# Kernel tuning notes

Measured on AMD Instinct MI355X. Metric: run time of the kernel, lower is better.

## Reference

```python
import jax, jax.numpy as jnp
import numpy as np

SIZES = [6890, 1723, 431, 108, 27]
P = [s + 1 for s in SIZES]  # padding vertex at each level
SPIRAL = 9
ENC_IN = [3, 16, 32, 64]; ENC_OUT = [16, 32, 64, 128]
DEC_IN = [128, 64, 32, 32, 16]; DEC_OUT = [64, 32, 32, 16, 3]
LATENT = 128
B = 64


def setup_inputs() -> dict:
    ks = iter(jax.random.split(jax.random.key(0), 80))
    def nrm(shape, scale=1.0):
        return jax.random.normal(next(ks), shape, dtype=jnp.float32) * scale
    inp = {'x': nrm((B, P[0], 3))}
    for l in range(4):
        inp['S%d' % l] = jax.random.randint(next(ks), (P[l], SPIRAL), 0, P[l], dtype=jnp.int32)
        inp['D%d' % l] = nrm((P[l + 1], P[l]), float(1.0 / np.sqrt(P[l])))
        inp['U%d' % l] = nrm((P[l], P[l + 1]), float(1.0 / np.sqrt(P[l + 1])))
    for i, (ci, co) in enumerate(zip(ENC_IN, ENC_OUT)):
        inp['W_e%d' % i] = nrm((ci * SPIRAL, co), float(1.0 / np.sqrt(ci * SPIRAL)))
        inp['b_e%d' % i] = nrm((co,), 0.02)
    inp['W_fe'] = nrm((P[4] * ENC_OUT[-1], LATENT), float(1.0 / np.sqrt(P[4] * ENC_OUT[-1])))
    inp['b_fe'] = nrm((LATENT,), 0.02)
    inp['W_fd'] = nrm((LATENT, P[4] * DEC_IN[0]), float(1.0 / np.sqrt(LATENT)))
    inp['b_fd'] = nrm((P[4] * DEC_IN[0],), 0.02)
    for i, (ci, co) in enumerate(zip(DEC_IN, DEC_OUT)):
        inp['W_d%d' % i] = nrm((ci * SPIRAL, co), float(1.0 / np.sqrt(ci * SPIRAL)))
        inp['b_d%d' % i] = nrm((co,), 0.02)
    return inp


def _sconv(x, idx, W, b, act):
    # spiral gather: x[B,P,F], idx[P,S] -> [B,P,S*F]; Linear + activation + zero last (padding) vertex
    Bn, Pn, F = x.shape
    g = x[:, idx, :].reshape(Bn, Pn, -1)
    y = act(g @ W + b)
    return y.at[:, -1, :].set(0.0)


def _forward(x, S, D, U, We, be, W_fe, b_fe, W_fd, b_fd, Wd, bd):
    elu = jax.nn.elu
    h = x
    for i in range(4):  # encoder: spiral conv then downsample
        h = _sconv(h, S[i], We[i], be[i], elu)
        h = jnp.einsum('pq,bqf->bpf', D[i], h)
    z = h.reshape(h.shape[0], -1) @ W_fe + b_fe
    h = (z @ W_fd + b_fd).reshape(z.shape[0], P[4], DEC_IN[0])
    for i in range(4):  # decoder: upsample then spiral conv
        h = jnp.einsum('pq,bqf->bpf', U[3 - i], h)
        h = _sconv(h, S[3 - i], Wd[i], bd[i], elu)
    h = _sconv(h, S[0], Wd[4], bd[4], lambda v: v)  # final identity-activation conv to xyz
    return h, z


def reference(x, S0, S1, S2, S3, D0, D1, D2, D3, U0, U1, U2, U3,
              W_e0, b_e0, W_e1, b_e1, W_e2, b_e2, W_e3, b_e3,
              W_fe, b_fe, W_fd, b_fd,
              W_d0, b_d0, W_d1, b_d1, W_d2, b_d2, W_d3, b_d3, W_d4, b_d4):
    return _forward(x, [S0, S1, S2, S3], [D0, D1, D2, D3], [U0, U1, U2, U3],
                    [W_e0, W_e1, W_e2, W_e3], [b_e0, b_e1, b_e2, b_e3],
                    W_fe, b_fe, W_fd, b_fd,
                    [W_d0, W_d1, W_d2, W_d3, W_d4], [b_d0, b_d1, b_d2, b_d3, b_d4])
```

## Files before the change

kernel.cpp:

```cpp
#include <hip/hip_runtime.h>
#include <math.h>

typedef unsigned short u16;
typedef _Float16 f16;
typedef __attribute__((ext_vector_type(8))) _Float16 f16x8;
typedef __attribute__((ext_vector_type(4))) float f32x4;
typedef float4 __attribute__((aligned(4))) float4u;

constexpr int P0 = 6891, P1 = 1724, P2 = 432, P3 = 109, P4 = 28;
constexpr int P0p = 6912;

constexpr size_t OFF_ZB   = 0;
constexpr size_t OFF_MD0  = OFF_ZB   + 256;
constexpr size_t OFF_MU0  = OFF_MD0  + (size_t)1792 * 6912 * 2;
constexpr size_t OFF_MD1  = OFF_MU0  + (size_t)6912 * 1792 * 2;
constexpr size_t OFF_MU1  = OFF_MD1  + (size_t)512 * 1792 * 2;
constexpr size_t OFF_MD2  = OFF_MU1  + (size_t)1792 * 512 * 2;
constexpr size_t OFF_MU2  = OFF_MD2  + (size_t)128 * 512 * 2;
constexpr size_t OFF_MD3  = OFF_MU2  + (size_t)512 * 128 * 2;
constexpr size_t OFF_MU3  = OFF_MD3  + (size_t)128 * 128 * 2;
constexpr size_t OFF_WE1  = OFF_MU3  + (size_t)128 * 128 * 2;
constexpr size_t OFF_WE2  = OFF_WE1  + (size_t)32 * 192 * 2;
constexpr size_t OFF_WE3  = OFF_WE2  + (size_t)64 * 320 * 2;
constexpr size_t OFF_WD0  = OFF_WE3  + (size_t)128 * 576 * 2;
constexpr size_t OFF_WD1  = OFF_WD0  + (size_t)64 * 1152 * 2;
constexpr size_t OFF_WD2  = OFF_WD1  + (size_t)32 * 576 * 2;
constexpr size_t OFF_WD3  = OFF_WD2  + (size_t)32 * 320 * 2;
constexpr size_t OFF_WT0  = OFF_WD3  + (size_t)16 * 320 * 2;
constexpr size_t OFF_XT   = OFF_WT0  + (size_t)16 * 128 * 2;
constexpr size_t OFF_FCP  = OFF_XT   + (size_t)6912 * 64 * 8 * 2;
constexpr size_t OFF_B0   = OFF_FCP  + (size_t)28 * 8192 * 4;
constexpr size_t OFF_B1   = OFF_B0   + (size_t)1024 * 6912 * 2;
constexpr size_t OFF_PB   = OFF_B1   + (size_t)6912 * 2048 * 2;
constexpr size_t OFF_END  = OFF_PB   + (size_t)14680064;

constexpr int CN_MD0 = 1792 * 864, CN_MU0 = 6912 * 224, CN_MD1 = 512 * 224,
              CN_MU1 = 1792 * 64, CN_MD2 = 128 * 64, CN_MU2 = 512 * 16,
              CN_MD3 = 128 * 16, CN_MU3 = 128 * 16,
              CN_W1 = 32 * 24, CN_W2 = 64 * 40, CN_W3 = 128 * 72,
              CN_V0 = 64 * 144, CN_V1 = 32 * 72, CN_V2 = 32 * 40, CN_V3 = 16 * 40,
              CN_W0 = 16 * 16, CN_XT = 6912 * 64, CN_ZB = 32;
constexpr int CN_TOTAL = CN_MD0 + CN_MU0 + CN_MD1 + CN_MU1 + CN_MD2 + CN_MU2 +
                         CN_MD3 + CN_MU3 + CN_W1 + CN_W2 + CN_W3 + CN_V0 + CN_V1 +
                         CN_V2 + CN_V3 + CN_W0 + CN_XT + CN_ZB;

__device__ __forceinline__ u16 f2h(float v) {
  f16 h = (f16)v;
  return __builtin_bit_cast(u16, h);
}
__device__ __forceinline__ float h2f(u16 u) {
  return (float)__builtin_bit_cast(f16, u);
}
__device__ __forceinline__ float eluf(float v) { return v > 0.f ? v : expm1f(v); }

__device__ __forceinline__ void gload16(const void* g, void* lds) {
  __builtin_amdgcn_global_load_lds(
      (const __attribute__((address_space(1))) unsigned int*)g,
      (__attribute__((address_space(3))) unsigned int*)lds, 16, 0, 0);
}

struct PrepSrc {
  const float *D0, *U0, *D1, *U1, *D2, *U2, *D3, *U3;
  const float *We1, *We2, *We3, *Wd0, *Wd1, *Wd2, *Wd3;
  const float *We0, *x;
};

__device__ __forceinline__ void conv_m_item(const float* __restrict__ M, u16* __restrict__ out,
                                            int idx, int P, int Q, int Qpad) {
  int cpr = Qpad >> 3;
  int p = idx / cpr, cq = idx - p * cpr;
  int w0 = (cq << 3) & ~63;
  int q0 = w0 + (((cq & 7) ^ (p & 7)) << 3);
  uint4 pk;
  if (p < P && q0 + 8 <= Q) {
    const float* s = M + (size_t)p * Q + q0;
    float4 va = *(const float4u*)s;
    float4 vb = *(const float4u*)(s + 4);
    pk.x = f2h(va.x) | ((unsigned)f2h(va.y) << 16);
    pk.y = f2h(va.z) | ((unsigned)f2h(va.w) << 16);
    pk.z = f2h(vb.x) | ((unsigned)f2h(vb.y) << 16);
    pk.w = f2h(vb.z) | ((unsigned)f2h(vb.w) << 16);
  } else {
    u16 v[8];
#pragma unroll
    for (int j = 0; j < 8; ++j) {
      int q = q0 + j;
      float f = (p < P && q < Q) ? M[(size_t)p * Q + q] : 0.f;
      v[j] = f2h(f);
    }
    pk.x = v[0] | ((unsigned)v[1] << 16); pk.y = v[2] | ((unsigned)v[3] << 16);
    pk.z = v[4] | ((unsigned)v[5] << 16); pk.w = v[6] | ((unsigned)v[7] << 16);
  }
  *(uint4*)(out + ((size_t)idx << 3)) = pk;
}

__device__ __forceinline__ void conv_w_item(const float* __restrict__ W, u16* __restrict__ out,
                                            int idx, int K, int F, int Kpad) {
  int cpr = Kpad >> 3;
  int co = idx / cpr, ck = idx - co * cpr;
  int w0 = (ck << 3) & ~63;
  int k0 = w0 + (((ck & 7) ^ (co & 7)) << 3);
  u16 v[8];
#pragma unroll
  for (int j = 0; j < 8; ++j) {
    int k = k0 + j;
    float f = (k < K) ? W[(size_t)k * F + co] : 0.f;
    v[j] = f2h(f);
  }
  uint4 pk;
  pk.x = v[0] | ((unsigned)v[1] << 16); pk.y = v[2] | ((unsigned)v[3] << 16);
  pk.z = v[4] | ((unsigned)v[5] << 16); pk.w = v[6] | ((unsigned)v[7] << 16);
  *(uint4*)(out + ((size_t)idx << 3)) = pk;
}

__device__ __forceinline__ void conv_w0_item(const float* __restrict__ W, u16* __restrict__ out,
                                             int idx) {
  int co = idx >> 4, ck = idx & 15;
  int w0 = (ck << 3) & ~63;
  int k0 = w0 + (((ck & 7) ^ (co & 7)) << 3);
  u16 v[8];
#pragma unroll
  for (int j = 0; j < 8; ++j) {
    int k = k0 + j;
    int s = k >> 3, c = k & 7;
    float f = (s < 9 && c < 3) ? W[(size_t)(s * 3 + c) * 16 + co] : 0.f;
    v[j] = f2h(f);
  }
  uint4 pk;
  pk.x = v[0] | ((unsigned)v[1] << 16); pk.y = v[2] | ((unsigned)v[3] << 16);
  pk.z = v[4] | ((unsigned)v[5] << 16); pk.w = v[6] | ((unsigned)v[7] << 16);
  *(uint4*)(out + ((size_t)idx << 3)) = pk;
}

__global__ __launch_bounds__(256) void kprep(PrepSrc a, char* __restrict__ ws) {
  int i = blockIdx.x * 256 + threadIdx.x;
  if (i >= CN_TOTAL) return;
  if (i < CN_MD0) { conv_m_item(a.D0, (u16*)(ws + OFF_MD0), i, P1, P0, 6912); return; }
  i -= CN_MD0;
  if (i < CN_MU0) { conv_m_item(a.U0, (u16*)(ws + OFF_MU0), i, P0, P1, 1792); return; }
  i -= CN_MU0;
  if (i < CN_XT) {
    u16* xt = (u16*)(ws + OFF_XT);
    int p = i >> 6, b = i & 63;
    float v0 = 0, v1 = 0, v2 = 0;
    if (p < P0) { const float* s = a.x + ((size_t)b * P0 + p) * 3; v0 = s[0]; v1 = s[1]; v2 = s[2]; }
    uint4 pk;
    pk.x = f2h(v0) | ((unsigned)f2h(v1) << 16);
    pk.y = f2h(v2);
    pk.z = 0; pk.w = 0;
    *(uint4*)(xt + ((size_t)i << 3)) = pk;
    return;
  }
  i -= CN_XT;
  if (i < CN_MD1) { conv_m_item(a.D1, (u16*)(ws + OFF_MD1), i, P2, P1, 1792); return; }
  i -= CN_MD1;
  if (i < CN_MU1) { conv_m_item(a.U1, (u16*)(ws + OFF_MU1), i, P1, P2, 512); return; }
  i -= CN_MU1;
  if (i < CN_MD2) { conv_m_item(a.D2, (u16*)(ws + OFF_MD2), i, P3, P2, 512); return; }
  i -= CN_MD2;
  if (i < CN_MU2) { conv_m_item(a.U2, (u16*)(ws + OFF_MU2), i, P2, P3, 128); return; }
  i -= CN_MU2;
  if (i < CN_MD3) { conv_m_item(a.D3, (u16*)(ws + OFF_MD3), i, P4, P3, 128); return; }
  i -= CN_MD3;
  if (i < CN_MU3) { conv_m_item(a.U3, (u16*)(ws + OFF_MU3), i, P3, P4, 128); return; }
  i -= CN_MU3;
  if (i < CN_W1) { conv_w_item(a.We1, (u16*)(ws + OFF_WE1), i, 144, 32, 192); return; }
  i -= CN_W1;
  if (i < CN_W2) { conv_w_item(a.We2, (u16*)(ws + OFF_WE2), i, 288, 64, 320); return; }
  i -= CN_W2;
  if (i < CN_W3) { conv_w_item(a.We3, (u16*)(ws + OFF_WE3), i, 576, 128, 576); return; }
  i -= CN_W3;
  if (i < CN_V0) { conv_w_item(a.Wd0, (u16*)(ws + OFF_WD0), i, 1152, 64, 1152); return; }
  i -= CN_V0;
  if (i < CN_V1) { conv_w_item(a.Wd1, (u16*)(ws + OFF_WD1), i, 576, 32, 576); return; }
  i -= CN_V1;
  if (i < CN_V2) { conv_w_item(a.Wd2, (u16*)(ws + OFF_WD2), i, 288, 32, 320); return; }
  i -= CN_V2;
  if (i < CN_V3) { conv_w_item(a.Wd3, (u16*)(ws + OFF_WD3), i, 288, 16, 320); return; }
  i -= CN_V3;
  if (i < CN_W0) { conv_w0_item(a.We0, (u16*)(ws + OFF_WT0), i); return; }
  i -= CN_W0;
  ((unsigned long long*)(ws + OFF_ZB))[i] = 0ull;
}

template <bool GATHER, int TN, int LOG_FIN, bool DO_ELU, int OUT_MODE = 0>
__global__ __launch_bounds__(256) void kgemm(const u16* __restrict__ Asrc, const u16* __restrict__ Bsrc,
                                             const int* __restrict__ S, const float* __restrict__ bias,
                                             u16* __restrict__ Cout, const u16* __restrict__ zb,
                                             int Kpad, int Pn, int PpadC, int N) {
  constexpr int NF = TN / 16;
  __shared__ u16 Ash[128 * 64];
  __shared__ u16 Bsh[TN * 64];
  __shared__ int Sl[16 * 12];

  const int t = threadIdx.x, w = t >> 6, l = t & 63;
  int p0, b0 = 0, n0 = 0;
  if (GATHER) { p0 = blockIdx.x * 16; b0 = blockIdx.y * 8; n0 = blockIdx.z * TN; }
  else        { p0 = blockIdx.x * 128; n0 = blockIdx.y * 128; }

  if constexpr (GATHER) {
    for (int i = t; i < 144; i += 256) {
      int pp = p0 + i / 9;
      Sl[(i / 9) * 12 + (i % 9)] = (pp < Pn) ? S[pp * 9 + (i % 9)] : 0;
    }
    __syncthreads();
  }

  const int NK = Kpad >> 6;
  int NKs, ks0;
  if constexpr (GATHER) { NKs = NK; ks0 = 0; }
  else                  { NKs = NK / gridDim.z; ks0 = blockIdx.z * NKs; }
  f32x4 acc[2][NF];
#pragma unroll
  for (int a = 0; a < 2; ++a)
#pragma unroll
    for (int b = 0; b < NF; ++b) acc[a][b] = (f32x4){0.f, 0.f, 0.f, 0.f};

  auto stage = [&](int ks) {
#pragma unroll
    for (int g0 = 0; g0 < 4; ++g0) {
      int g = g0 * 4 + w;
      int r = g * 8 + (l >> 3);
      const u16* src;
      if constexpr (GATHER) {
        int c = (l & 7) ^ (r & 7);
        int k = ks * 64 + c * 8;
        int s = k >> LOG_FIN;
        if (s < 9) {
          int kk = k & ((1 << LOG_FIN) - 1);
          int sv = Sl[(r & 15) * 12 + s];
          src = Asrc + (((size_t)(sv << 6) + b0 + (r >> 4)) << LOG_FIN) + kk;
        } else src = zb;
      } else {
        src = Asrc + (size_t)(p0 + r) * Kpad + ks * 64 + (l & 7) * 8;
      }
      gload16(src, &Ash[g * 512]);
    }
#pragma unroll
    for (int g0 = 0; g0 < (TN / 8 + 3) / 4; ++g0) {
      int g = g0 * 4 + w;
      if (g < TN / 8) {
        int r = g * 8 + (l >> 3);
        const u16* src = Bsrc + (size_t)(n0 + r) * Kpad + ks * 64 + (l & 7) * 8;
        gload16(src, &Bsh[g * 512]);
      }
    }
  };

  auto compute = [&]() {
#pragma unroll
    for (int kh = 0; kh < 2; ++kh) {
      f16x8 av[2], bv[NF];
#pragma unroll
      for (int mf = 0; mf < 2; ++mf) {
        int r = w * 32 + mf * 16 + (l & 15);
        int c = kh * 4 + (l >> 4);
        av[mf] = *(const f16x8*)&Ash[r * 64 + ((c ^ (r & 7)) << 3)];
      }
#pragma unroll
      for (int nf = 0; nf < NF; ++nf) {
        int r = nf * 16 + (l & 15);
        int c = kh * 4 + (l >> 4);
        bv[nf] = *(const f16x8*)&Bsh[r * 64 + ((c ^ (r & 7)) << 3)];
      }
#pragma unroll
      for (int mf = 0; mf < 2; ++mf)
#pragma unroll
        for (int nf = 0; nf < NF; ++nf)
          acc[mf][nf] = __builtin_amdgcn_mfma_f32_16x16x32_f16(av[mf], bv[nf], acc[mf][nf], 0, 0, 0);
    }
  };

  for (int i = 0; i < NKs; ++i) {
    stage(ks0 + i);
    __syncthreads();
    compute();
    __syncthreads();
  }

  if constexpr (GATHER && OUT_MODE == 1) {
    u16* T = &Ash[0];
    int co = l & 15;
    float bb = bias[co];
    int prow = (l >> 4) << 2;
#pragma unroll
    for (int mf = 0; mf < 2; ++mf) {
      int ncol = (w * 2 + mf) * 16 + co;
#pragma unroll
      for (int rg = 0; rg < 4; ++rg) {
        float v = acc[mf][0][rg] + bb;
        if (DO_ELU) v = eluf(v);
        if (p0 + prow + rg >= Pn - 1) v = 0.f;
        T[(prow + rg) * 136 + ncol] = f2h(v);
      }
    }
    __syncthreads();
    int r = t >> 4, c8 = (t & 15) << 3;
    uint4 pk = *(const uint4*)&T[r * 136 + c8];
    *(uint4*)(Cout + (size_t)(p0 + r) * (64 * TN) + (size_t)blockIdx.y * 128 + c8) = pk;
  } else if constexpr (GATHER) {
#pragma unroll
    for (int nf = 0; nf < NF; ++nf) {
      int co = n0 + nf * 16 + (l & 15);
      float bb = bias[co];
#pragma unroll
      for (int mf = 0; mf < 2; ++mf) {
        int b = b0 + w * 2 + mf;
        int n = b * N + co;
        int pbase = p0 + ((l >> 4) << 2);
        u16 hv[4];
#pragma unroll
        for (int rg = 0; rg < 4; ++rg) {
          float v = acc[mf][nf][rg] + bb;
          if (DO_ELU) v = eluf(v);
          if (pbase + rg >= Pn - 1) v = 0.f;
          hv[rg] = f2h(v);
        }
        int slot = ((pbase >> 3) & 7) ^ (n & 7);
        u16* dst = Cout + (size_t)n * PpadC + (pbase & ~63) + (slot << 3) + (pbase & 7);
        uint2 pk;
        pk.x = hv[0] | ((unsigned)hv[1] << 16);
        pk.y = hv[2] | ((unsigned)hv[3] << 16);
        *(uint2*)dst = pk;
      }
    }
  } else {
    u16* Cb = Cout + (size_t)blockIdx.z * ((size_t)gridDim.x * 128 * N);
#pragma unroll
    for (int mf = 0; mf < 2; ++mf) {
      int pb = p0 + w * 32 + mf * 16 + ((l >> 4) << 2);
#pragma unroll
      for (int nf = 0; nf < NF; ++nf) {
        int n = n0 + nf * 16 + (l & 15);
#pragma unroll
        for (int rg = 0; rg < 4; ++rg)
          Cb[(size_t)(pb + rg) * N + n] = f2h(acc[mf][nf][rg]);
      }
    }
  }
}

__global__ __launch_bounds__(256) void kred(const u16* __restrict__ part, u16* __restrict__ out,
                                            int mn8, int sk, size_t slice) {
  int i = blockIdx.x * 256 + threadIdx.x;
  if (i >= mn8) return;
  size_t base = (size_t)i * 8;
  float s[8] = {};
  for (int z = 0; z < sk; ++z) {
    uint4 u = *(const uint4*)(part + z * slice + base);
    s[0] += h2f((u16)u.x); s[1] += h2f((u16)(u.x >> 16));
    s[2] += h2f((u16)u.y); s[3] += h2f((u16)(u.y >> 16));
    s[4] += h2f((u16)u.z); s[5] += h2f((u16)(u.z >> 16));
    s[6] += h2f((u16)u.w); s[7] += h2f((u16)(u.w >> 16));
  }
  uint4 o;
  o.x = f2h(s[0]) | ((unsigned)f2h(s[1]) << 16);
  o.y = f2h(s[2]) | ((unsigned)f2h(s[3]) << 16);
  o.z = f2h(s[4]) | ((unsigned)f2h(s[5]) << 16);
  o.w = f2h(s[6]) | ((unsigned)f2h(s[7]) << 16);
  *(uint4*)(out + base) = o;
}

__global__ __launch_bounds__(256) void kfc_enc1(const u16* __restrict__ h, const float* __restrict__ W,
                                                float* __restrict__ partial) {
  __shared__ float hs[64][128];
  __shared__ float wsh[128][64];
  int p = blockIdx.x, nh = blockIdx.y, t = threadIdx.x;
  for (int i = t; i < 8192; i += 256) hs[i >> 7][i & 127] = h2f(h[(size_t)p * 8192 + i]);
  for (int i = t; i < 128 * 64; i += 256) {
    int kk = i >> 6, jj = i & 63;
    wsh[kk][jj] = W[(size_t)(p * 128 + kk) * 128 + nh * 64 + jj];
  }
  __syncthreads();
  int j = t & 63, bg = t >> 6;
  float acc[16] = {};
  for (int k = 0; k < 128; ++k) {
    float wv = wsh[k][j];
#pragma unroll
    for (int i = 0; i < 16; ++i) acc[i] = fmaf(hs[bg * 16 + i][k], wv, acc[i]);
  }
#pragma unroll
  for (int i = 0; i < 16; ++i)
    partial[((size_t)p * 64 + bg * 16 + i) * 128 + nh * 64 + j] = acc[i];
}

__global__ __launch_bounds__(256) void kfc_dec(const float* __restrict__ partial,
                                               const float* __restrict__ bfe, float* __restrict__ z,
                                               const float* __restrict__ W,
                                               const float* __restrict__ bias, u16* __restrict__ out) {
  __shared__ float zs[8][128];
  int t = threadIdx.x, b0 = blockIdx.y * 8;
  for (int i = t; i < 8 * 128; i += 256) {
    int bb = i >> 7, j = i & 127;
    float s = bfe[j];
    for (int p = 0; p < 28; ++p) s += partial[(size_t)p * 8192 + (b0 + bb) * 128 + j];
    zs[bb][j] = s;
    if (blockIdx.x == 0) z[(b0 + bb) * 128 + j] = s;
  }
  __syncthreads();
  int m = blockIdx.x * 256 + t;
  float bb = bias[m];
  float acc[8];
#pragma unroll
  for (int i = 0; i < 8; ++i) acc[i] = bb;
  for (int k = 0; k < 128; ++k) {
    float wv = W[(size_t)k * 3584 + m];
#pragma unroll
    for (int i = 0; i < 8; ++i) acc[i] = fmaf(zs[i][k], wv, acc[i]);
  }
  int p = m >> 7, f = m & 127;
  int slot0 = p >> 3;
#pragma unroll
  for (int i = 0; i < 8; ++i) {
    int n = (b0 + i) * 128 + f;
    int slot = slot0 ^ (n & 7);
    out[(size_t)n * 128 + (slot << 3) + (p & 7)] = f2h(acc[i]);
  }
}

__global__ __launch_bounds__(256) void kfinal(const u16* __restrict__ x, const int* __restrict__ S,
                                              const float* __restrict__ W, const float* __restrict__ bias,
                                              float* __restrict__ out) {
  __shared__ float Wl[432];
  __shared__ int Sl[64 * 9];
  int t = threadIdx.x;
  for (int i = t; i < 432; i += 256) Wl[i] = W[i];
  int pblk = blockIdx.x * 64;
  for (int i = t; i < 64 * 9; i += 256) {
    int pp = pblk + i / 9;
    Sl[i] = (pp < P0) ? S[pp * 9 + (i % 9)] : 0;
  }
  __syncthreads();
  int lane = t & 63, w = t >> 6;
  int p = pblk + lane;
  float b0v = bias[0], b1v = bias[1], b2v = bias[2];
  int idxs[9];
#pragma unroll
  for (int s = 0; s < 9; ++s) idxs[s] = Sl[lane * 9 + s];
#pragma unroll
  for (int bi = 0; bi < 2; ++bi) {
    int b = blockIdx.y * 8 + w * 2 + bi;
    float a0 = b0v, a1 = b1v, a2 = b2v;
    for (int s = 0; s < 9; ++s) {
      const f16x8* xr = (const f16x8*)(x + ((size_t)idxs[s] * 64 + b) * 16);
      f16x8 v0 = xr[0], v1 = xr[1];
#pragma unroll
      for (int j = 0; j < 8; ++j) {
        float xv = (float)v0[j];
        a0 = fmaf(xv, Wl[(s * 16 + j) * 3 + 0], a0);
        a1 = fmaf(xv, Wl[(s * 16 + j) * 3 + 1], a1);
        a2 = fmaf(xv, Wl[(s * 16 + j) * 3 + 2], a2);
      }
#pragma unroll
      for (int j = 0; j < 8; ++j) {
        float xv = (float)v1[j];
        a0 = fmaf(xv, Wl[(s * 16 + j + 8) * 3 + 0], a0);
        a1 = fmaf(xv, Wl[(s * 16 + j + 8) * 3 + 1], a1);
        a2 = fmaf(xv, Wl[(s * 16 + j + 8) * 3 + 2], a2);
      }
    }
    if (p < P0) {
      float* o = out + ((size_t)b * P0 + p) * 3;
      if (p == P0 - 1) { o[0] = 0.f; o[1] = 0.f; o[2] = 0.f; }
      else             { o[0] = a0;  o[1] = a1;  o[2] = a2; }
    }
  }
}

extern "C" void kernel_launch(void* const* d_in, const int* in_sizes, int n_in,
                              void* d_out, int out_size, void* d_ws, size_t ws_size,
                              hipStream_t stream) {
  (void)in_sizes; (void)n_in; (void)out_size;

  const float* x   = (const float*)d_in[0];
  const int*   S0  = (const int*)d_in[1];
  const float* D0  = (const float*)d_in[2];
  const float* U0  = (const float*)d_in[3];
  const int*   S1  = (const int*)d_in[4];
  const float* D1  = (const float*)d_in[5];
  const float* U1  = (const float*)d_in[6];
  const int*   S2  = (const int*)d_in[7];
  const float* D2  = (const float*)d_in[8];
  const float* U2  = (const float*)d_in[9];
  const int*   S3  = (const int*)d_in[10];
  const float* D3  = (const float*)d_in[11];
  const float* U3  = (const float*)d_in[12];
  const float* We0 = (const float*)d_in[13]; const float* be0 = (const float*)d_in[14];
  const float* We1 = (const float*)d_in[15]; const float* be1 = (const float*)d_in[16];
  const float* We2 = (const float*)d_in[17]; const float* be2 = (const float*)d_in[18];
  const float* We3 = (const float*)d_in[19]; const float* be3 = (const float*)d_in[20];
  const float* Wfe = (const float*)d_in[21]; const float* bfe = (const float*)d_in[22];
  const float* Wfd = (const float*)d_in[23]; const float* bfd = (const float*)d_in[24];
  const float* Wd0 = (const float*)d_in[25]; const float* bd0 = (const float*)d_in[26];
  const float* Wd1 = (const float*)d_in[27]; const float* bd1 = (const float*)d_in[28];
  const float* Wd2 = (const float*)d_in[29]; const float* bd2 = (const float*)d_in[30];
  const float* Wd3 = (const float*)d_in[31]; const float* bd3 = (const float*)d_in[32];
  const float* Wd4 = (const float*)d_in[33]; const float* bd4 = (const float*)d_in[34];

  char* ws = (char*)d_ws;
  u16*   zb   = (u16*)(ws + OFF_ZB);
  u16*   MbD0 = (u16*)(ws + OFF_MD0); u16* MbU0 = (u16*)(ws + OFF_MU0);
  u16*   MbD1 = (u16*)(ws + OFF_MD1); u16* MbU1 = (u16*)(ws + OFF_MU1);
  u16*   MbD2 = (u16*)(ws + OFF_MD2); u16* MbU2 = (u16*)(ws + OFF_MU2);
  u16*   MbD3 = (u16*)(ws + OFF_MD3); u16* MbU3 = (u16*)(ws + OFF_MU3);
  u16*   Wte1 = (u16*)(ws + OFF_WE1); u16* Wte2 = (u16*)(ws + OFF_WE2);
  u16*   Wte3 = (u16*)(ws + OFF_WE3); u16* Wtd0 = (u16*)(ws + OFF_WD0);
  u16*   Wtd1 = (u16*)(ws + OFF_WD1); u16* Wtd2 = (u16*)(ws + OFF_WD2);
  u16*   Wtd3 = (u16*)(ws + OFF_WD3); u16* Wt0  = (u16*)(ws + OFF_WT0);
  u16*   xt16 = (u16*)(ws + OFF_XT);
  float* fcp  = (float*)(ws + OFF_FCP);
  u16*   B0   = (u16*)(ws + OFF_B0);
  u16*   B1   = (u16*)(ws + OFF_B1);
  u16*   Pbuf = (u16*)(ws + OFF_PB);
  const bool sk = OFF_END <= ws_size;

  float* out_h = (float*)d_out;
  float* out_z = out_h + (size_t)64 * P0 * 3;

  auto cdiv = [](int a, int b) { return (a + b - 1) / b; };
  dim3 blk(256);

  auto rs = [&](const u16* Mb, const u16* Bin, int Mtiles, int Ntiles, int Kpad, int N, int SK) {
    if (sk && SK > 1) {
      kgemm<false, 128, 0, false><<<dim3(Mtiles, Ntiles, SK), blk, 0, stream>>>(
          Mb, Bin, nullptr, nullptr, Pbuf, zb, Kpad, 0, 0, N);
      int mn = Mtiles * 128 * N;
      kred<<<cdiv(mn / 8, 256), blk, 0, stream>>>(Pbuf, B1, mn / 8, SK, (size_t)mn);
    } else {
      kgemm<false, 128, 0, false><<<dim3(Mtiles, Ntiles), blk, 0, stream>>>(
          Mb, Bin, nullptr, nullptr, B1, zb, Kpad, 0, 0, N);
    }
  };

  PrepSrc ps{D0, U0, D1, U1, D2, U2, D3, U3, We1, We2, We3, Wd0, Wd1, Wd2, Wd3, We0, x};
  kprep<<<cdiv(CN_TOTAL, 256), blk, 0, stream>>>(ps, ws);

  kgemm<true, 16, 3, true><<<dim3(432, 8), blk, 0, stream>>>(xt16, Wt0, S0, be0, B0, zb, 128, P0, P0p, 16);
  rs(MbD0, B0, 14, 8, 6912, 1024, 4);
  kgemm<true, 32, 4, true><<<dim3(112, 8), blk, 0, stream>>>(B1, Wte1, S1, be1, B0, zb, 192, P1, 1792, 32);
  rs(MbD1, B0, 4, 16, 1792, 2048, 7);
  kgemm<true, 64, 5, true><<<dim3(32, 8), blk, 0, stream>>>(B1, Wte2, S2, be2, B0, zb, 320, P2, 512, 64);
  rs(MbD2, B0, 1, 32, 512, 4096, 4);
  kgemm<true, 64, 6, true><<<dim3(8, 8, 2), blk, 0, stream>>>(B1, Wte3, S3, be3, B0, zb, 576, P3, 128, 128);
  rs(MbD3, B0, 1, 64, 128, 8192, 1);

  kfc_enc1<<<dim3(28, 2), blk, 0, stream>>>(B1, Wfe, fcp);
  kfc_dec<<<dim3(14, 8), blk, 0, stream>>>(fcp, bfe, out_z, Wfd, bfd, B0);

  rs(MbU3, B0, 1, 64, 128, 8192, 1);
  kgemm<true, 32, 7, true><<<dim3(8, 8, 2), blk, 0, stream>>>(B1, Wtd0, S3, bd0, B0, zb, 1152, P3, 128, 64);
  rs(MbU2, B0, 4, 32, 128, 4096, 1);
  kgemm<true, 32, 6, true><<<dim3(32, 8), blk, 0, stream>>>(B1, Wtd1, S2, bd1, B0, zb, 576, P2, 512, 32);
  rs(MbU1, B0, 14, 16, 512, 2048, 2);
  kgemm<true, 32, 5, true><<<dim3(112, 8), blk, 0, stream>>>(B1, Wtd2, S1, bd2, B0, zb, 320, P1, 1792, 32);
  rs(MbU0, B0, 54, 16, 1792, 2048, 1);
  kgemm<true, 16, 5, true, 1><<<dim3(432, 8), blk, 0, stream>>>(B1, Wtd3, S0, bd3, B0, zb, 320, P0, 0, 16);

  kfinal<<<dim3(108, 8), blk, 0, stream>>>(B0, S0, Wd4, bd4, out_h);
}
```

Measured before the change: 411.7 us.

## Add 256x256 triple-buffered MFMA GEMM kernel for final U0 upsample

Replaces the generic rs() launch for the largest upsample (U0, 6912x1792 by 1792x2048) with a dedicated 512-thread kernel. It uses 256x256 output tiles, three LDS stages filled by direct global-to-LDS loads, and 8x4 MFMA fragments per wave. The U0 matrix is now packed without the XOR swizzle so the new kernel can read rows linearly, while B keeps its swizzled layout. The large tile and 128 accumulator vectors per thread raise register pressure and allow only one block per CU, trading occupancy for data reuse.

```diff
diff --git a/kernel.cpp b/kernel.cpp
--- a/kernel.cpp
+++ b/kernel.cpp
@@ -66,11 +66,16 @@
 };
 
 __device__ __forceinline__ void conv_m_item(const float* __restrict__ M, u16* __restrict__ out,
-                                            int idx, int P, int Q, int Qpad) {
+                                            int idx, int P, int Q, int Qpad, bool swz) {
   int cpr = Qpad >> 3;
   int p = idx / cpr, cq = idx - p * cpr;
-  int w0 = (cq << 3) & ~63;
-  int q0 = w0 + (((cq & 7) ^ (p & 7)) << 3);
+  int q0;
+  if (swz) {
+    int w0 = (cq << 3) & ~63;
+    q0 = w0 + (((cq & 7) ^ (p & 7)) << 3);
+  } else {
+    q0 = cq << 3;
+  }
   uint4 pk;
   if (p < P && q0 + 8 <= Q) {
     const float* s = M + (size_t)p * Q + q0;
@@ -135,9 +140,9 @@
 __global__ __launch_bounds__(256) void kprep(PrepSrc a, char* __restrict__ ws) {
   int i = blockIdx.x * 256 + threadIdx.x;
   if (i >= CN_TOTAL) return;
-  if (i < CN_MD0) { conv_m_item(a.D0, (u16*)(ws + OFF_MD0), i, P1, P0, 6912); return; }
+  if (i < CN_MD0) { conv_m_item(a.D0, (u16*)(ws + OFF_MD0), i, P1, P0, 6912, true); return; }
   i -= CN_MD0;
-  if (i < CN_MU0) { conv_m_item(a.U0, (u16*)(ws + OFF_MU0), i, P0, P1, 1792); return; }
+  if (i < CN_MU0) { conv_m_item(a.U0, (u16*)(ws + OFF_MU0), i, P0, P1, 1792, false); return; }
   i -= CN_MU0;
   if (i < CN_XT) {
     u16* xt = (u16*)(ws + OFF_XT);
@@ -152,17 +157,17 @@
     return;
   }
   i -= CN_XT;
-  if (i < CN_MD1) { conv_m_item(a.D1, (u16*)(ws + OFF_MD1), i, P2, P1, 1792); return; }
+  if (i < CN_MD1) { conv_m_item(a.D1, (u16*)(ws + OFF_MD1), i, P2, P1, 1792, true); return; }
   i -= CN_MD1;
-  if (i < CN_MU1) { conv_m_item(a.U1, (u16*)(ws + OFF_MU1), i, P1, P2, 512); return; }
+  if (i < CN_MU1) { conv_m_item(a.U1, (u16*)(ws + OFF_MU1), i, P1, P2, 512, true); return; }
   i -= CN_MU1;
-  if (i < CN_MD2) { conv_m_item(a.D2, (u16*)(ws + OFF_MD2), i, P3, P2, 512); return; }
+  if (i < CN_MD2) { conv_m_item(a.D2, (u16*)(ws + OFF_MD2), i, P3, P2, 512, true); return; }
   i -= CN_MD2;
-  if (i < CN_MU2) { conv_m_item(a.U2, (u16*)(ws + OFF_MU2), i, P2, P3, 128); return; }
+  if (i < CN_MU2) { conv_m_item(a.U2, (u16*)(ws + OFF_MU2), i, P2, P3, 128, true); return; }
   i -= CN_MU2;
-  if (i < CN_MD3) { conv_m_item(a.D3, (u16*)(ws + OFF_MD3), i, P4, P3, 128); return; }
+  if (i < CN_MD3) { conv_m_item(a.D3, (u16*)(ws + OFF_MD3), i, P4, P3, 128, true); return; }
   i -= CN_MD3;
-  if (i < CN_MU3) { conv_m_item(a.U3, (u16*)(ws + OFF_MU3), i, P3, P4, 128); return; }
+  if (i < CN_MU3) { conv_m_item(a.U3, (u16*)(ws + OFF_MU3), i, P3, P4, 128, true); return; }
   i -= CN_MU3;
   if (i < CN_W1) { conv_w_item(a.We1, (u16*)(ws + OFF_WE1), i, 144, 32, 192); return; }
   i -= CN_W1;
@@ -181,6 +186,81 @@
   if (i < CN_W0) { conv_w0_item(a.We0, (u16*)(ws + OFF_WT0), i); return; }
   i -= CN_W0;
   ((unsigned long long*)(ws + OFF_ZB))[i] = 0ull;
+}
+
+__global__ __launch_bounds__(512, 1) void kgemm8(const u16* __restrict__ A, const u16* __restrict__ B,
+                                                 u16* __restrict__ C, int Kpad, int N) {
+  __shared__ u16 lds[3 * 16384];
+  const int t = threadIdx.x, l = t & 63;
+  const int w = t >> 6, wr = w >> 2, wc = w & 3;
+  const int pt = blockIdx.x * 256, nt = blockIdx.y * 256;
+  const int NK = Kpad >> 5;
+
+  f32x4 acc[8][4];
+#pragma unroll
+  for (int a = 0; a < 8; ++a)
+#pragma unroll
+    for (int b = 0; b < 4; ++b) acc[a][b] = (f32x4){0.f, 0.f, 0.f, 0.f};
+
+  auto stage = [&](int q, int ks) {
+#pragma unroll
+    for (int j = 0; j < 2; ++j) {
+      int s = t + j * 512;
+      int row = (s & 15) | ((s >> 6) << 4);
+      int kc = (s >> 4) & 3;
+      const u16* src = A + (size_t)(pt + row) * Kpad + ks * 32 + kc * 8;
+      gload16(src, &lds[q * 16384 + (s & ~63) * 8]);
+    }
+#pragma unroll
+    for (int j = 0; j < 2; ++j) {
+      int s = t + j * 512;
+      int nrow = (s & 15) | ((s >> 6) << 4);
+      int kc = (s >> 4) & 3;
+      int lc = ((ks & 1) << 2) + kc;
+      int slot = lc ^ (nrow & 7);
+      const u16* src = B + (size_t)(nt + nrow) * Kpad + ((ks >> 1) << 6) + (slot << 3);
+      gload16(src, &lds[q * 16384 + 8192 + (s & ~63) * 8]);
+    }
+  };
+
+  stage(0, 0);
+  if (NK > 1) stage(1, 1);
+
+  for (int k = 0; k < NK; ++k) {
+    asm volatile("s_waitcnt vmcnt(4)" ::: "memory");
+    __builtin_amdgcn_s_barrier();
+    __builtin_amdgcn_sched_barrier(0);
+    int q = k % 3;
+    if (k + 2 < NK) stage((k + 2) % 3, k + 2);
+    const u16* bufA = &lds[q * 16384];
+    const u16* bufB = bufA + 8192;
+    f16x8 av[8], bv[4];
+#pragma unroll
+    for (int mf = 0; mf < 8; ++mf)
+      av[mf] = *(const f16x8*)&bufA[(wr * 8 + mf) * 512 + l * 8];
+#pragma unroll
+    for (int nf = 0; nf < 4; ++nf)
+      bv[nf] = *(const f16x8*)&bufB[(wc * 4 + nf) * 512 + l * 8];
+    __builtin_amdgcn_s_setprio(1);
+#pragma unroll
+    for (int mf = 0; mf < 8; ++mf)
+#pragma unroll
+      for (int nf = 0; nf < 4; ++nf)
+        acc[mf][nf] = __builtin_amdgcn_mfma_f32_16x16x32_f16(av[mf], bv[nf], acc[mf][nf], 0, 0, 0);
+    __builtin_amdgcn_s_setprio(0);
+  }
+
+#pragma unroll
+  for (int mf = 0; mf < 8; ++mf) {
+    int prow = pt + wr * 128 + mf * 16 + ((l >> 4) << 2);
+#pragma unroll
+    for (int nf = 0; nf < 4; ++nf) {
+      int ncol = nt + wc * 64 + nf * 16 + (l & 15);
+#pragma unroll
+      for (int rg = 0; rg < 4; ++rg)
+        C[(size_t)(prow + rg) * N + ncol] = f2h(acc[mf][nf][rg]);
+    }
+  }
 }
 
 template <bool GATHER, int TN, int LOG_FIN, bool DO_ELU, int OUT_MODE = 0>
@@ -553,7 +633,7 @@
   kgemm<true, 32, 6, true><<<dim3(32, 8), blk, 0, stream>>>(B1, Wtd1, S2, bd1, B0, zb, 576, P2, 512, 32);
   rs(MbU1, B0, 14, 16, 512, 2048, 2);
   kgemm<true, 32, 5, true><<<dim3(112, 8), blk, 0, stream>>>(B1, Wtd2, S1, bd2, B0, zb, 320, P1, 1792, 32);
-  rs(MbU0, B0, 54, 16, 1792, 2048, 1);
+  kgemm8<<<dim3(27, 8), dim3(512), 0, stream>>>(MbU0, B0, B1, 1792, 2048);
   kgemm<true, 16, 5, true, 1><<<dim3(432, 8), blk, 0, stream>>>(B1, Wtd3, S0, bd3, B0, zb, 320, P0, 0, 16);
 
   kfinal<<<dim3(108, 8), blk, 0, stream>>>(B0, S0, Wd4, bd4, out_h);
```

New measurement: 395.8 us (median of 2 runs). -3.8%, faster.
